# Performance work log

Hardware: AMD Instinct MI355X
Metric: run time of the kernel (lower is better)

## Reference

```python
import jax, jax.numpy as jnp
import numpy as np

EPS = 1e-5
NEG_SLOPE = 0.01  # torch LeakyReLU default


def setup_inputs() -> dict:
    key = jax.random.key(0)
    k1, k2 = jax.random.split(key)
    B, C, N, OUT = 4, 256, 4096, 256
    stdv = 1.0 / np.sqrt(OUT)
    x = jax.random.normal(k1, (B, C, N), dtype=jnp.float32)
    W = jax.random.uniform(k2, (C, OUT), dtype=jnp.float32, minval=-stdv, maxval=stdv)
    gamma = jnp.ones((OUT,), dtype=jnp.float32)
    beta = jnp.zeros((OUT,), dtype=jnp.float32)
    return {"x": x, "W": W, "gamma": gamma, "beta": beta}


def reference(x, W, gamma, beta):
    # x: [B, C, N] -> xt: [B, N, C]
    xt = jnp.transpose(x, (0, 2, 1))
    # adjacency: softmax over last dim of [B, N, N] self-similarity (L2=False path)
    scores = jnp.einsum('bnc,bmc->bnm', xt, xt)
    adj = jax.nn.softmax(scores, axis=-1)
    # support: [B, N, OUT]
    support = jnp.einsum('bnc,co->bno', xt, W)
    # output: [B, OUT, N]
    out = jnp.transpose(jnp.einsum('bnm,bmo->bno', adj, support), (0, 2, 1))
    y = jnp.where(out >= 0, out, NEG_SLOPE * out)  # LeakyReLU
    # BatchNorm1d (training mode): per-channel stats over batch and spatial dims
    mean = jnp.mean(y, axis=(0, 2), keepdims=True)
    var = jnp.mean(jnp.square(y - mean), axis=(0, 2), keepdims=True)
    y_hat = (y - mean) * jax.lax.rsqrt(var + EPS)
    return gamma[None, :, None] * y_hat + beta[None, :, None]
```

## Files before the change

kernel.cpp:

```cpp
#include <hip/hip_runtime.h>

typedef _Float16 f16;
typedef _Float16 f16x2 __attribute__((ext_vector_type(2)));
typedef _Float16 f16x8 __attribute__((ext_vector_type(8)));
typedef float f32x4 __attribute__((ext_vector_type(4)));

#define B_   4
#define C_   256
#define N_   4096
#define OUT_ 256

__device__ __forceinline__ void gld_lds16(const f16* g, f16* l) {
    __builtin_amdgcn_global_load_lds(
        (const __attribute__((address_space(1))) void*)g,
        (__attribute__((address_space(3))) void*)l, 16, 0, 0);
}

__global__ __launch_bounds__(256) void k_prep(const float* __restrict__ x,
                                              const float* __restrict__ W,
                                              f16* __restrict__ xt,
                                              f16* __restrict__ Wt,
                                              float* __restrict__ stats) {
    int bid = blockIdx.x;
    int t = threadIdx.x;
    if (bid < 1024) {
        int b  = bid >> 8;
        int ct = (bid >> 6) & 3;
        int nt = bid & 63;
        int c0 = ct * 64, n0 = nt * 64;
        __shared__ float tile[64][65];
        int nl = t & 63;
        int r0 = t >> 6;
        #pragma unroll
        for (int i = 0; i < 16; ++i) {
            int cl = i * 4 + r0;
            tile[cl][nl] = x[((b * C_ + c0 + cl) * N_) + n0 + nl];
        }
        __syncthreads();
        #pragma unroll
        for (int i = 0; i < 16; ++i) {
            int nl2 = i * 4 + r0;
            int cl2 = nl;
            xt[((b * N_ + n0 + nl2) * C_) + c0 + cl2] = (f16)tile[cl2][nl2];
        }
    } else {
        int wb = bid - 1024;
        #pragma unroll
        for (int i = 0; i < 4; ++i) {
            int idx = wb * 1024 + i * 256 + t;
            int c = idx >> 8, o = idx & 255;
            Wt[o * C_ + c] = (f16)W[idx];
        }
        if (wb < 2) stats[wb * 256 + t] = 0.f;
    }
}

__global__ __launch_bounds__(256) void k_support(const f16* __restrict__ xt,
                                                 const f16* __restrict__ Wt,
                                                 f16* __restrict__ supT) {
    int bid0 = blockIdx.x;
    int bid = (bid0 & 7) * 128 + (bid0 >> 3);
    int b  = bid >> 8;
    int ot = (bid >> 6) & 3;
    int mt = bid & 63;
    int o0 = ot * 64, m0 = mt * 64;
    __shared__ __align__(16) f16 Ws[64][264];
    __shared__ __align__(16) f16 Xs[64][264];
    int t = threadIdx.x;
    int wave = t >> 6, lane = t & 63, q = lane >> 4, l15 = lane & 15;
    #pragma unroll
    for (int p = 0; p < 8; ++p) {
        int idx = p * 256 + t;
        int row = idx >> 5, ch = (idx & 31) * 8;
        *(uint4*)&Ws[row][ch] = *(const uint4*)&Wt[(o0 + row) * C_ + ch];
        *(uint4*)&Xs[row][ch] = *(const uint4*)&xt[((b * N_) + m0 + row) * C_ + ch];
    }
    __syncthreads();
    f32x4 acc[4] = {};
    #pragma unroll
    for (int kk = 0; kk < 8; ++kk) {
        f16x8 a = *(f16x8*)&Ws[16 * wave + l15][kk * 32 + q * 8];
        #pragma unroll
        for (int ct = 0; ct < 4; ++ct) {
            f16x8 bb = *(f16x8*)&Xs[16 * ct + l15][kk * 32 + q * 8];
            acc[ct] = __builtin_amdgcn_mfma_f32_16x16x32_f16(a, bb, acc[ct], 0, 0, 0);
        }
    }
    #pragma unroll
    for (int ct = 0; ct < 4; ++ct)
        #pragma unroll
        for (int r = 0; r < 4; ++r) {
            int og = o0 + 16 * wave + q * 4 + r;
            int mg = m0 + 16 * ct + l15;
            supT[((b * OUT_ + og) * N_) + mg] = (f16)acc[ct][r];
        }
}

__global__ __launch_bounds__(256) __attribute__((amdgpu_waves_per_eu(2, 2)))
void k_flash(const f16* __restrict__ xt,
             const f16* __restrict__ supT,
             f16* __restrict__ Op,
             float* __restrict__ Ml) {
    int bid0 = blockIdx.x;
    int wg = (bid0 & 7) * 64 + (bid0 >> 3);
    int h  = wg >> 8;
    int b  = (wg >> 6) & 3;
    int n0 = (wg & 63) * 64;

    __shared__ __align__(16) f16 KsL[2][64 * 256];
    __shared__ __align__(16) f16 Ps[64][72];
    __shared__ float Al[64];

    int t = threadIdx.x;
    int wave = t >> 6, lane = t & 63, q = lane >> 4, l15 = lane & 15;

    const f16* qbase = xt + ((size_t)(b * N_) + n0 + 16 * wave + l15) * C_;
    f16x8 qf[8];
    #pragma unroll
    for (int kk = 0; kk < 8; ++kk)
        qf[kk] = *(const f16x8*)&qbase[kk * 32 + q * 8];

    f32x4 oacc[4][4] = {};
    float m_run = -1e30f, l_run = 0.f;

    const f16* kbase = xt + (size_t)b * N_ * C_;
    int c16 = (lane & 31) * 8;
    int rhalf = lane >> 5;
    int soff[8];
    #pragma unroll
    for (int j = 0; j < 8; ++j) {
        int row = wave * 16 + j * 2 + rhalf;
        soff[j] = row * 256 + (c16 ^ ((row & 7) << 3));
    }
    int swr = (l15 & 7) << 3;

    {
        const f16* kt = kbase + (size_t)(h * 2048) * C_;
        #pragma unroll
        for (int j = 0; j < 8; ++j)
            gld_lds16(kt + soff[j], &KsL[0][wave * 4096 + j * 512]);
    }

    int cur = 0;
    for (int it = 0; it < 32; ++it) {
        int m0 = h * 2048 + it * 64;

        __syncthreads();

        f16x8 vf[2][4];
        const f16* vb = supT + ((size_t)(b * OUT_) + 64 * wave + l15) * N_ + m0 + q * 8;
        #pragma unroll
        for (int ks = 0; ks < 2; ++ks)
            #pragma unroll
            for (int ot = 0; ot < 4; ++ot)
                vf[ks][ot] = *(const f16x8*)&vb[(size_t)(16 * ot) * N_ + ks * 32];

        if (it < 31) {
            const f16* kt = kbase + (size_t)(m0 + 64) * C_;
            #pragma unroll
            for (int j = 0; j < 8; ++j)
                gld_lds16(kt + soff[j], &KsL[cur ^ 1][wave * 4096 + j * 512]);
        }

        f32x4 sacc[4] = {};
        __builtin_amdgcn_s_setprio(1);
        #pragma unroll
        for (int kk = 0; kk < 8; ++kk) {
            int col = (kk * 32 + q * 8) ^ swr;
            #pragma unroll
            for (int mt = 0; mt < 4; ++mt) {
                f16x8 kf = *(f16x8*)&KsL[cur][(16 * mt + l15) * 256 + col];
                sacc[mt] = __builtin_amdgcn_mfma_f32_16x16x32_f16(kf, qf[kk], sacc[mt], 0, 0, 0);
            }
        }
        __builtin_amdgcn_s_setprio(0);

        float mt0 = fmaxf(fmaxf(sacc[0][0], sacc[0][1]), fmaxf(sacc[0][2], sacc[0][3]));
        float mt1 = fmaxf(fmaxf(sacc[1][0], sacc[1][1]), fmaxf(sacc[1][2], sacc[1][3]));
        float mt2 = fmaxf(fmaxf(sacc[2][0], sacc[2][1]), fmaxf(sacc[2][2], sacc[2][3]));
        float mt3 = fmaxf(fmaxf(sacc[3][0], sacc[3][1]), fmaxf(sacc[3][2], sacc[3][3]));
        float mx = fmaxf(fmaxf(mt0, mt1), fmaxf(mt2, mt3));
        mx = fmaxf(mx, __shfl_xor(mx, 16));
        mx = fmaxf(mx, __shfl_xor(mx, 32));
        float mnew = fmaxf(m_run, mx);
        float alpha = __expf(m_run - mnew);
        m_run = mnew;

        float p[4][4];
        #pragma unroll
        for (int mt = 0; mt < 4; ++mt)
            #pragma unroll
            for (int r = 0; r < 4; ++r)
                p[mt][r] = __expf(sacc[mt][r] - mnew);
        float s0 = (p[0][0] + p[0][1]) + (p[0][2] + p[0][3]);
        float s1 = (p[1][0] + p[1][1]) + (p[1][2] + p[1][3]);
        float s2 = (p[2][0] + p[2][1]) + (p[2][2] + p[2][3]);
        float s3 = (p[3][0] + p[3][1]) + (p[3][2] + p[3][3]);
        float sum = (s0 + s1) + (s2 + s3);
        sum += __shfl_xor(sum, 16);
        sum += __shfl_xor(sum, 32);
        l_run = l_run * alpha + sum;

        #pragma unroll
        for (int mt = 0; mt < 4; ++mt)
            #pragma unroll
            for (int j = 0; j < 2; ++j) {
                f16x2 pp = { (f16)p[mt][2 * j], (f16)p[mt][2 * j + 1] };
                *(f16x2*)&Ps[16 * wave + l15][16 * mt + 4 * q + 2 * j] = pp;
            }
        if (lane < 16) Al[16 * wave + lane] = alpha;

        asm volatile("s_waitcnt lgkmcnt(0)" ::: "memory");
        __builtin_amdgcn_s_barrier();
        __builtin_amdgcn_sched_barrier(0);

        float4 av[4];
        #pragma unroll
        for (int nt = 0; nt < 4; ++nt)
            av[nt] = *(const float4*)&Al[16 * nt + 4 * q];
        #pragma unroll
        for (int nt = 0; nt < 4; ++nt)
            #pragma unroll
            for (int ot = 0; ot < 4; ++ot)
                #pragma unroll
                for (int r = 0; r < 4; ++r)
                    oacc[nt][ot][r] *= ((const float*)&av[nt])[r];

        __builtin_amdgcn_s_setprio(1);
        #pragma unroll
        for (int ks = 0; ks < 2; ++ks) {
            f16x8 af[4];
            #pragma unroll
            for (int nt = 0; nt < 4; ++nt)
                af[nt] = *(f16x8*)&Ps[16 * nt + l15][ks * 32 + q * 8];
            #pragma unroll
            for (int nt = 0; nt < 4; ++nt)
                #pragma unroll
                for (int ot = 0; ot < 4; ++ot)
                    oacc[nt][ot] = __builtin_amdgcn_mfma_f32_16x16x32_f16(af[nt], vf[ks][ot], oacc[nt][ot], 0, 0, 0);
        }
        __builtin_amdgcn_s_setprio(0);
        cur ^= 1;
    }

    __syncthreads();
    if (lane < 16) Al[16 * wave + lane] = 1.0f / l_run;
    __syncthreads();
    float4 lv[4];
    #pragma unroll
    for (int nt = 0; nt < 4; ++nt)
        lv[nt] = *(const float4*)&Al[16 * nt + 4 * q];

    f16* Obase = Op + (size_t)wg * (64 * 256);
    #pragma unroll
    for (int nt = 0; nt < 4; ++nt)
        #pragma unroll
        for (int ot = 0; ot < 4; ++ot)
            #pragma unroll
            for (int r = 0; r < 4; ++r) {
                int n = 16 * nt + q * 4 + r;
                int o = 64 * wave + 16 * ot + l15;
                Obase[n * 256 + o] = (f16)(oacc[nt][ot][r] * ((const float*)&lv[nt])[r]);
            }
    float* Mlb = Ml + (size_t)wg * 128;
    if (lane < 16) {
        Mlb[16 * wave + lane] = m_run;
        Mlb[64 + 16 * wave + lane] = l_run;
    }
}

__global__ __launch_bounds__(256) void k_merge(const f16* __restrict__ Op,
                                               const float* __restrict__ Ml,
                                               float* __restrict__ out,
                                               float* __restrict__ stats) {
    int bid = blockIdx.x;
    int b  = bid >> 6;
    int n0 = (bid & 63) * 64;
    int t = threadIdx.x;
    const f16* O1 = Op + (size_t)bid * (64 * 256);
    const f16* O2 = Op + (size_t)(bid + 256) * (64 * 256);
    const float* Ml1 = Ml + (size_t)bid * 128;
    const float* Ml2 = Ml + (size_t)(bid + 256) * 128;
    __shared__ float c1s[64], c2s[64];
    __shared__ float tile[256][65];
    if (t < 64) {
        float m1 = Ml1[t], l1 = Ml1[64 + t];
        float m2 = Ml2[t], l2 = Ml2[64 + t];
        float m = fmaxf(m1, m2);
        float w1 = __expf(m1 - m) * l1;
        float w2 = __expf(m2 - m) * l2;
        float inv = 1.0f / (w1 + w2);
        c1s[t] = w1 * inv;
        c2s[t] = w2 * inv;
    }
    __syncthreads();
    int p2 = (t & 127) * 2;
    int nh = (t >> 7) * 32;
    float s0 = 0.f, s1 = 0.f, ss0 = 0.f, ss1 = 0.f;
    #pragma unroll 8
    for (int j = 0; j < 32; ++j) {
        int n = nh + j;
        f16x2 u1 = *(const f16x2*)&O1[n * 256 + p2];
        f16x2 u2 = *(const f16x2*)&O2[n * 256 + p2];
        float c1 = c1s[n], c2 = c2s[n];
        float v0 = c1 * (float)u1[0] + c2 * (float)u2[0];
        float v1 = c1 * (float)u1[1] + c2 * (float)u2[1];
        v0 = v0 >= 0.f ? v0 : 0.01f * v0;
        v1 = v1 >= 0.f ? v1 : 0.01f * v1;
        s0 += v0; ss0 += v0 * v0;
        s1 += v1; ss1 += v1 * v1;
        tile[p2][n] = v0;
        tile[p2 + 1][n] = v1;
    }
    atomicAdd(&stats[p2], s0);
    atomicAdd(&stats[p2 + 1], s1);
    atomicAdd(&stats[256 + p2], ss0);
    atomicAdd(&stats[257 + p2], ss1);
    __syncthreads();
    int w = t >> 6, lane = t & 63;
    float* dst = out + (size_t)(b * OUT_) * N_ + n0;
    #pragma unroll
    for (int k = 0; k < 64; ++k) {
        int o = 64 * w + k;
        dst[(size_t)o * N_ + lane] = tile[o][lane];
    }
}

__global__ __launch_bounds__(256) void k_bnapply(float* __restrict__ y,
                                                 const float* __restrict__ stats,
                                                 const float* __restrict__ gamma,
                                                 const float* __restrict__ beta) {
    int idx = blockIdx.x * 256 + threadIdx.x;
    int o = (idx >> 10) & 255;
    float mean = stats[o] * (1.0f / 16384.0f);
    float var = stats[256 + o] * (1.0f / 16384.0f) - mean * mean;
    float rstd = rsqrtf(var + 1e-5f);
    float g = gamma[o] * rstd;
    float bta = beta[o] - mean * g;
    float4 v = ((const float4*)y)[idx];
    v.x = v.x * g + bta;
    v.y = v.y * g + bta;
    v.z = v.z * g + bta;
    v.w = v.w * g + bta;
    ((float4*)y)[idx] = v;
}

extern "C" void kernel_launch(void* const* d_in, const int* in_sizes, int n_in,
                              void* d_out, int out_size, void* d_ws, size_t ws_size,
                              hipStream_t stream) {
    const float* x     = (const float*)d_in[0];
    const float* W     = (const float*)d_in[1];
    const float* gamma = (const float*)d_in[2];
    const float* beta  = (const float*)d_in[3];
    float* out = (float*)d_out;

    f16* xt    = (f16*)d_ws;
    f16* supT  = xt + (size_t)B_ * N_ * C_;
    f16* Wt    = supT + (size_t)B_ * N_ * OUT_;
    f16* Op    = Wt + C_ * OUT_;
    float* Ml  = (float*)(Op + (size_t)2 * 256 * 64 * 256);
    float* stats = Ml + 512 * 128;

    k_prep<<<1088, 256, 0, stream>>>(x, W, xt, Wt, stats);
    k_support<<<1024, 256, 0, stream>>>(xt, Wt, supT);
    k_flash<<<512, 256, 0, stream>>>(xt, supT, Op, Ml);
    k_merge<<<256, 256, 0, stream>>>(Op, Ml, out, stats);
    k_bnapply<<<4096, 256, 0, stream>>>(out, stats, gamma, beta);
}
```

Baseline: 214.5 us.

## Software-pipeline QK^T of next tile with softmax and PV of current tile

Restructures the flash-attention loop so the score MFMAs for tile it+1 are issued in the same phase as the PV MFMAs for tile it, with a prologue computing the first scores. K tiles are prefetched two steps ahead into the double-buffered LDS, and V fragments for the next tile are loaded at the end of each iteration. The goal is to overlap softmax/exp work and memory latency with matrix-core work. In exchange it needs more registers (snew plus sacc live alongside oacc), and the vmcnt(0) wait plus an extra barrier per iteration could stall the loop.

```diff
diff --git a/kernel.cpp b/kernel.cpp
--- a/kernel.cpp
+++ b/kernel.cpp
@@ -134,47 +134,46 @@
     }
     int swr = (l15 & 7) << 3;
 
+    const f16* vbbase = supT + ((size_t)(b * OUT_) + 64 * wave + l15) * N_ + q * 8;
+
     {
         const f16* kt = kbase + (size_t)(h * 2048) * C_;
         #pragma unroll
         for (int j = 0; j < 8; ++j)
             gld_lds16(kt + soff[j], &KsL[0][wave * 4096 + j * 512]);
     }
-
-    int cur = 0;
-    for (int it = 0; it < 32; ++it) {
-        int m0 = h * 2048 + it * 64;
-
-        __syncthreads();
-
-        f16x8 vf[2][4];
-        const f16* vb = supT + ((size_t)(b * OUT_) + 64 * wave + l15) * N_ + m0 + q * 8;
+    asm volatile("s_waitcnt vmcnt(0) lgkmcnt(0)" ::: "memory");
+    __builtin_amdgcn_s_barrier();
+    __builtin_amdgcn_sched_barrier(0);
+    {
+        const f16* kt = kbase + (size_t)(h * 2048 + 64) * C_;
+        #pragma unroll
+        for (int j = 0; j < 8; ++j)
+            gld_lds16(kt + soff[j], &KsL[1][wave * 4096 + j * 512]);
+    }
+    f16x8 vf[2][4];
+    {
+        const f16* vb = vbbase + h * 2048;
         #pragma unroll
         for (int ks = 0; ks < 2; ++ks)
             #pragma unroll
             for (int ot = 0; ot < 4; ++ot)
                 vf[ks][ot] = *(const f16x8*)&vb[(size_t)(16 * ot) * N_ + ks * 32];
-
-        if (it < 31) {
-            const f16* kt = kbase + (size_t)(m0 + 64) * C_;
-            #pragma unroll
-            for (int j = 0; j < 8; ++j)
-                gld_lds16(kt + soff[j], &KsL[cur ^ 1][wave * 4096 + j * 512]);
-        }
-
-        f32x4 sacc[4] = {};
-        __builtin_amdgcn_s_setprio(1);
-        #pragma unroll
-        for (int kk = 0; kk < 8; ++kk) {
-            int col = (kk * 32 + q * 8) ^ swr;
-            #pragma unroll
-            for (int mt = 0; mt < 4; ++mt) {
-                f16x8 kf = *(f16x8*)&KsL[cur][(16 * mt + l15) * 256 + col];
-                sacc[mt] = __builtin_amdgcn_mfma_f32_16x16x32_f16(kf, qf[kk], sacc[mt], 0, 0, 0);
-            }
-        }
-        __builtin_amdgcn_s_setprio(0);
-
+    }
+    f32x4 sacc[4] = {};
+    __builtin_amdgcn_s_setprio(1);
+    #pragma unroll
+    for (int kk = 0; kk < 8; ++kk) {
+        int col = (kk * 32 + q * 8) ^ swr;
+        #pragma unroll
+        for (int mt = 0; mt < 4; ++mt) {
+            f16x8 kf = *(f16x8*)&KsL[0][(16 * mt + l15) * 256 + col];
+            sacc[mt] = __builtin_amdgcn_mfma_f32_16x16x32_f16(kf, qf[kk], sacc[mt], 0, 0, 0);
+        }
+    }
+    __builtin_amdgcn_s_setprio(0);
+
+    for (int it = 0; it < 32; ++it) {
         float mt0 = fmaxf(fmaxf(sacc[0][0], sacc[0][1]), fmaxf(sacc[0][2], sacc[0][3]));
         float mt1 = fmaxf(fmaxf(sacc[1][0], sacc[1][1]), fmaxf(sacc[1][2], sacc[1][3]));
         float mt2 = fmaxf(fmaxf(sacc[2][0], sacc[2][1]), fmaxf(sacc[2][2], sacc[2][3]));
@@ -210,14 +209,39 @@
             }
         if (lane < 16) Al[16 * wave + lane] = alpha;
 
-        asm volatile("s_waitcnt lgkmcnt(0)" ::: "memory");
+        asm volatile("s_waitcnt vmcnt(0) lgkmcnt(0)" ::: "memory");
         __builtin_amdgcn_s_barrier();
         __builtin_amdgcn_sched_barrier(0);
 
+        if (it < 30) {
+            const f16* kt = kbase + (size_t)(h * 2048 + (it + 2) * 64) * C_;
+            f16* kdst = &KsL[it & 1][0];
+            #pragma unroll
+            for (int j = 0; j < 8; ++j)
+                gld_lds16(kt + soff[j], kdst + wave * 4096 + j * 512);
+        }
+
         float4 av[4];
         #pragma unroll
         for (int nt = 0; nt < 4; ++nt)
             av[nt] = *(const float4*)&Al[16 * nt + 4 * q];
+
+        __builtin_amdgcn_s_setprio(1);
+        if (it < 31) {
+            const f16* kcur = &KsL[(it + 1) & 1][0];
+            f32x4 snew[4] = {};
+            #pragma unroll
+            for (int kk = 0; kk < 8; ++kk) {
+                int col = (kk * 32 + q * 8) ^ swr;
+                #pragma unroll
+                for (int mt = 0; mt < 4; ++mt) {
+                    f16x8 kf = *(f16x8*)&kcur[(16 * mt + l15) * 256 + col];
+                    snew[mt] = __builtin_amdgcn_mfma_f32_16x16x32_f16(kf, qf[kk], snew[mt], 0, 0, 0);
+                }
+            }
+            #pragma unroll
+            for (int mt = 0; mt < 4; ++mt) sacc[mt] = snew[mt];
+        }
         #pragma unroll
         for (int nt = 0; nt < 4; ++nt)
             #pragma unroll
@@ -225,8 +249,6 @@
                 #pragma unroll
                 for (int r = 0; r < 4; ++r)
                     oacc[nt][ot][r] *= ((const float*)&av[nt])[r];
-
-        __builtin_amdgcn_s_setprio(1);
         #pragma unroll
         for (int ks = 0; ks < 2; ++ks) {
             f16x8 af[4];
@@ -240,7 +262,19 @@
                     oacc[nt][ot] = __builtin_amdgcn_mfma_f32_16x16x32_f16(af[nt], vf[ks][ot], oacc[nt][ot], 0, 0, 0);
         }
         __builtin_amdgcn_s_setprio(0);
-        cur ^= 1;
+
+        if (it < 31) {
+            const f16* vb = vbbase + h * 2048 + (it + 1) * 64;
+            #pragma unroll
+            for (int ks = 0; ks < 2; ++ks)
+                #pragma unroll
+                for (int ot = 0; ot < 4; ++ot)
+                    vf[ks][ot] = *(const f16x8*)&vb[(size_t)(16 * ot) * N_ + ks * 32];
+        }
+
+        asm volatile("s_waitcnt lgkmcnt(0)" ::: "memory");
+        __builtin_amdgcn_s_barrier();
+        __builtin_amdgcn_sched_barrier(0);
     }
 
     __syncthreads();
```

Result: slower. 227.4 us (+6.0%).

## Switch flash QK^T to 32x32x16 MFMA with 2x2 wave tiling

Applied to the files above, without the earlier changes.

The score computation now uses 32x32x16 MFMA tiles, with the four waves arranged as 2x2 over query and key halves instead of each wave owning 16 query rows against all 64 keys. Each wave issues one 32-row K fragment load per k-chunk instead of four, and uses permlane32 swaps for the in-wave reductions. The aim is fewer LDS reads and MFMA issues per score tile. The cost is that row max and row sum must now be combined across wave pairs through shared memory, which adds an extra barrier per iteration, and the query fragments take more registers (16 f16x8).

```diff
diff --git a/kernel.cpp b/kernel.cpp
--- a/kernel.cpp
+++ b/kernel.cpp
@@ -2,8 +2,11 @@
 
 typedef _Float16 f16;
 typedef _Float16 f16x2 __attribute__((ext_vector_type(2)));
+typedef _Float16 f16x4 __attribute__((ext_vector_type(4)));
 typedef _Float16 f16x8 __attribute__((ext_vector_type(8)));
 typedef float f32x4 __attribute__((ext_vector_type(4)));
+typedef float f32x16 __attribute__((ext_vector_type(16)));
+typedef int i32x2 __attribute__((ext_vector_type(2)));
 
 #define B_   4
 #define C_   256
@@ -14,6 +17,10 @@
     __builtin_amdgcn_global_load_lds(
         (const __attribute__((address_space(1))) void*)g,
         (__attribute__((address_space(3))) void*)l, 16, 0, 0);
+}
+
+__device__ __forceinline__ i32x2 perm32(float x) {
+    return __builtin_amdgcn_permlane32_swap(__float_as_int(x), __float_as_int(x), false, false);
 }
 
 __global__ __launch_bounds__(256) void k_prep(const float* __restrict__ x,
@@ -110,15 +117,20 @@
     __shared__ __align__(16) f16 KsL[2][64 * 256];
     __shared__ __align__(16) f16 Ps[64][72];
     __shared__ float Al[64];
+    __shared__ float SmX[2][2][32];
+    __shared__ float SmS[2][2][32];
 
     int t = threadIdx.x;
-    int wave = t >> 6, lane = t & 63, q = lane >> 4, l15 = lane & 15;
-
-    const f16* qbase = xt + ((size_t)(b * N_) + n0 + 16 * wave + l15) * C_;
-    f16x8 qf[8];
-    #pragma unroll
-    for (int kk = 0; kk < 8; ++kk)
-        qf[kk] = *(const f16x8*)&qbase[kk * 32 + q * 8];
+    int wave = t >> 6, lane = t & 63;
+    int q = lane >> 4, l15 = lane & 15;
+    int l31 = lane & 31, hi = lane >> 5;
+    int nh = wave & 1, mh = wave >> 1;
+
+    const f16* qbase = xt + ((size_t)(b * N_) + n0 + 32 * nh + l31) * C_ + 8 * hi;
+    f16x8 qf[16];
+    #pragma unroll
+    for (int kc = 0; kc < 16; ++kc)
+        qf[kc] = *(const f16x8*)&qbase[16 * kc];
 
     f32x4 oacc[4][4] = {};
     float m_run = -1e30f, l_run = 0.f;
@@ -132,7 +144,9 @@
         int row = wave * 16 + j * 2 + rhalf;
         soff[j] = row * 256 + (c16 ^ ((row & 7) << 3));
     }
-    int swr = (l15 & 7) << 3;
+    int swr = (l31 & 7) << 3;
+
+    const f16* vbbase = supT + ((size_t)(b * OUT_) + 64 * wave + l15) * N_ + q * 8;
 
     {
         const f16* kt = kbase + (size_t)(h * 2048) * C_;
@@ -148,7 +162,7 @@
         __syncthreads();
 
         f16x8 vf[2][4];
-        const f16* vb = supT + ((size_t)(b * OUT_) + 64 * wave + l15) * N_ + m0 + q * 8;
+        const f16* vb = vbbase + m0;
         #pragma unroll
         for (int ks = 0; ks < 2; ++ks)
             #pragma unroll
@@ -162,57 +176,68 @@
                 gld_lds16(kt + soff[j], &KsL[cur ^ 1][wave * 4096 + j * 512]);
         }
 
-        f32x4 sacc[4] = {};
+        f32x16 sacc = {};
+        const f16* krow = &KsL[cur][(32 * mh + l31) * 256];
         __builtin_amdgcn_s_setprio(1);
         #pragma unroll
-        for (int kk = 0; kk < 8; ++kk) {
-            int col = (kk * 32 + q * 8) ^ swr;
-            #pragma unroll
-            for (int mt = 0; mt < 4; ++mt) {
-                f16x8 kf = *(f16x8*)&KsL[cur][(16 * mt + l15) * 256 + col];
-                sacc[mt] = __builtin_amdgcn_mfma_f32_16x16x32_f16(kf, qf[kk], sacc[mt], 0, 0, 0);
-            }
+        for (int kc = 0; kc < 16; ++kc) {
+            int col = (16 * kc + 8 * hi) ^ swr;
+            f16x8 kf = *(const f16x8*)&krow[col];
+            sacc = __builtin_amdgcn_mfma_f32_32x32x16_f16(kf, qf[kc], sacc, 0, 0, 0);
         }
         __builtin_amdgcn_s_setprio(0);
 
-        float mt0 = fmaxf(fmaxf(sacc[0][0], sacc[0][1]), fmaxf(sacc[0][2], sacc[0][3]));
-        float mt1 = fmaxf(fmaxf(sacc[1][0], sacc[1][1]), fmaxf(sacc[1][2], sacc[1][3]));
-        float mt2 = fmaxf(fmaxf(sacc[2][0], sacc[2][1]), fmaxf(sacc[2][2], sacc[2][3]));
-        float mt3 = fmaxf(fmaxf(sacc[3][0], sacc[3][1]), fmaxf(sacc[3][2], sacc[3][3]));
-        float mx = fmaxf(fmaxf(mt0, mt1), fmaxf(mt2, mt3));
-        mx = fmaxf(mx, __shfl_xor(mx, 16));
-        mx = fmaxf(mx, __shfl_xor(mx, 32));
-        float mnew = fmaxf(m_run, mx);
-        float alpha = __expf(m_run - mnew);
-        m_run = mnew;
-
-        float p[4][4];
-        #pragma unroll
-        for (int mt = 0; mt < 4; ++mt)
-            #pragma unroll
-            for (int r = 0; r < 4; ++r)
-                p[mt][r] = __expf(sacc[mt][r] - mnew);
-        float s0 = (p[0][0] + p[0][1]) + (p[0][2] + p[0][3]);
-        float s1 = (p[1][0] + p[1][1]) + (p[1][2] + p[1][3]);
-        float s2 = (p[2][0] + p[2][1]) + (p[2][2] + p[2][3]);
-        float s3 = (p[3][0] + p[3][1]) + (p[3][2] + p[3][3]);
-        float sum = (s0 + s1) + (s2 + s3);
-        sum += __shfl_xor(sum, 16);
-        sum += __shfl_xor(sum, 32);
-        l_run = l_run * alpha + sum;
-
-        #pragma unroll
-        for (int mt = 0; mt < 4; ++mt)
-            #pragma unroll
-            for (int j = 0; j < 2; ++j) {
-                f16x2 pp = { (f16)p[mt][2 * j], (f16)p[mt][2 * j + 1] };
-                *(f16x2*)&Ps[16 * wave + l15][16 * mt + 4 * q + 2 * j] = pp;
-            }
-        if (lane < 16) Al[16 * wave + lane] = alpha;
+        float a0 = fmaxf(fmaxf(sacc[0], sacc[1]), fmaxf(sacc[2], sacc[3]));
+        float a1 = fmaxf(fmaxf(sacc[4], sacc[5]), fmaxf(sacc[6], sacc[7]));
+        float a2 = fmaxf(fmaxf(sacc[8], sacc[9]), fmaxf(sacc[10], sacc[11]));
+        float a3 = fmaxf(fmaxf(sacc[12], sacc[13]), fmaxf(sacc[14], sacc[15]));
+        float pmax = fmaxf(fmaxf(a0, a1), fmaxf(a2, a3));
+        {
+            i32x2 r = perm32(pmax);
+            pmax = fmaxf(__int_as_float(r[0]), __int_as_float(r[1]));
+        }
+        if (lane < 32) SmX[mh][nh][l31] = pmax;
 
         asm volatile("s_waitcnt lgkmcnt(0)" ::: "memory");
         __builtin_amdgcn_s_barrier();
         __builtin_amdgcn_sched_barrier(0);
+
+        float omax = SmX[mh ^ 1][nh][l31];
+        float mnew = fmaxf(m_run, fmaxf(pmax, omax));
+        float alpha = __expf(m_run - mnew);
+        m_run = mnew;
+
+        float p[16];
+        #pragma unroll
+        for (int r = 0; r < 16; ++r)
+            p[r] = __expf(sacc[r] - mnew);
+        float s0 = (p[0] + p[1]) + (p[2] + p[3]);
+        float s1 = (p[4] + p[5]) + (p[6] + p[7]);
+        float s2 = (p[8] + p[9]) + (p[10] + p[11]);
+        float s3 = (p[12] + p[13]) + (p[14] + p[15]);
+        float wsum = (s0 + s1) + (s2 + s3);
+        {
+            i32x2 r = perm32(wsum);
+            wsum = __int_as_float(r[0]) + __int_as_float(r[1]);
+        }
+
+        #pragma unroll
+        for (int g = 0; g < 4; ++g) {
+            f16x4 pk = { (f16)p[4 * g], (f16)p[4 * g + 1],
+                         (f16)p[4 * g + 2], (f16)p[4 * g + 3] };
+            *(f16x4*)&Ps[32 * nh + l31][32 * mh + 8 * g + 4 * hi] = pk;
+        }
+        if (lane < 32) {
+            SmS[mh][nh][l31] = wsum;
+            if (mh == 0) Al[32 * nh + l31] = alpha;
+        }
+
+        asm volatile("s_waitcnt lgkmcnt(0)" ::: "memory");
+        __builtin_amdgcn_s_barrier();
+        __builtin_amdgcn_sched_barrier(0);
+
+        float psum = SmS[mh ^ 1][nh][l31];
+        l_run = l_run * alpha + wsum + psum;
 
         float4 av[4];
         #pragma unroll
@@ -244,7 +269,7 @@
     }
 
     __syncthreads();
-    if (lane < 16) Al[16 * wave + lane] = 1.0f / l_run;
+    if (wave < 2 && lane < 32) Al[wave * 32 + lane] = 1.0f / l_run;
     __syncthreads();
     float4 lv[4];
     #pragma unroll
@@ -263,9 +288,9 @@
                 Obase[n * 256 + o] = (f16)(oacc[nt][ot][r] * ((const float*)&lv[nt])[r]);
             }
     float* Mlb = Ml + (size_t)wg * 128;
-    if (lane < 16) {
-        Mlb[16 * wave + lane] = m_run;
-        Mlb[64 + 16 * wave + lane] = l_run;
+    if (wave < 2 && lane < 32) {
+        Mlb[wave * 32 + lane] = m_run;
+        Mlb[64 + wave * 32 + lane] = l_run;
     }
 }
 
```

Result: no change. 213.9 us (-0.3%).
